# Kernel tuning notes

Measured on AMD Instinct MI355X. Metric: run time of the kernel, lower is better.

The kernel has to match this reference:

```python
import jax, jax.numpy as jnp
import numpy as np

NUM_STREAMS = 4
SINKHORN_ITERS = 10
TAU = 0.05


def sinkhorn_project(logits):
    # logits: [S, S] -> near doubly-stochastic matrix, log-domain Sinkhorn
    S = logits.shape[0]
    scaled = logits / TAU
    scaled = scaled - jnp.max(scaled)
    log_marginal = jnp.full((S,), -jnp.log(jnp.asarray(S, scaled.dtype)), dtype=scaled.dtype)
    u = jnp.zeros((S,), dtype=scaled.dtype)
    v = jnp.zeros((S,), dtype=scaled.dtype)

    def body(_, uv):
        u, v = uv
        u = log_marginal - jax.nn.logsumexp(scaled + v[None, :], axis=1)
        v = log_marginal - jax.nn.logsumexp(scaled + u[:, None], axis=0)
        return (u, v)

    u, v = jax.lax.fori_loop(0, SINKHORN_ITERS, body, (u, v))
    return jnp.exp(scaled + u[:, None] + v[None, :]) * S


def setup_inputs() -> dict:
    key = jax.random.key(0)
    k1, k2, k3, k4 = jax.random.split(key, 4)
    B_eff, T, D = 32, 2048, 1024  # B_eff = B * NUM_STREAMS
    streams = jax.random.normal(k1, (B_eff, T, D), dtype=jnp.float32)
    # params initialized like the module (base logit scale 8.0)
    base = 8.0
    h_res_logits = jnp.full((NUM_STREAMS, NUM_STREAMS), -base, dtype=jnp.float32)
    h_res_logits = h_res_logits.at[jnp.arange(NUM_STREAMS), jnp.arange(NUM_STREAMS)].set(0.0)
    h_res_logits = h_res_logits + 0.1 * jax.random.normal(k2, (NUM_STREAMS, NUM_STREAMS), dtype=jnp.float32)
    h_pre_logits = jnp.full((NUM_STREAMS,), -base, dtype=jnp.float32).at[0].set(0.0)
    h_pre_logits = h_pre_logits + 0.1 * jax.random.normal(k3, (NUM_STREAMS,), dtype=jnp.float32)
    h_post_logits = jnp.full((NUM_STREAMS,), -base, dtype=jnp.float32).at[0].set(0.0)
    h_post_logits = h_post_logits + 0.1 * jax.random.normal(k4, (NUM_STREAMS,), dtype=jnp.float32)
    return {"streams": streams, "h_res_logits": h_res_logits,
            "h_pre_logits": h_pre_logits, "h_post_logits": h_post_logits}


def reference(streams, h_res_logits, h_pre_logits, h_post_logits):
    S = NUM_STREAMS
    BS, T, D = streams.shape
    B = BS // S
    # [B*S, T, D] -> [B, T, S, D]
    x = streams.reshape(B, S, T, D).transpose(0, 2, 1, 3)
    h_res = sinkhorn_project(h_res_logits)           # [S, S]
    h_pre = jax.nn.softmax(h_pre_logits)             # [S]
    h_post = jax.nn.softmax(h_post_logits)           # [S]
    residual_mixed = jnp.einsum('ij,btjd->btid', h_res, x)   # [B, T, S, D]
    branch_input = jnp.einsum('s,btsd->btd', h_pre, x)       # [B, T, D]
    branch_output = branch_input  # branch_fn = identity
    out = residual_mixed + branch_output[:, :, None, :] * h_post[None, None, :, None]
    # [B, T, S, D] -> [B*S, T, D]
    return out.transpose(0, 2, 1, 3).reshape(B * S, T, D)
```

## Files before the change

### kernel.cpp

```cpp
#include <hip/hip_runtime.h>
#include <math.h>

#define NSTREAMS 4
#define SINKHORN_ITERS 10
#define TAU 0.05f
#define BATCH 8
#define N4_SHIFT 19
#define TOTAL_ITEMS (BATCH << N4_SHIFT)

typedef float f32x4 __attribute__((ext_vector_type(4)));

__global__ void coeff_kernel(const float* __restrict__ res_logits,
                             const float* __restrict__ pre_logits,
                             const float* __restrict__ post_logits,
                             float* __restrict__ coeffs) {
    if (threadIdx.x != 0 || blockIdx.x != 0) return;

    float scaled[NSTREAMS][NSTREAMS];
    float mx = -INFINITY;
    #pragma unroll
    for (int i = 0; i < NSTREAMS; ++i)
        #pragma unroll
        for (int j = 0; j < NSTREAMS; ++j) {
            float sv = res_logits[i * NSTREAMS + j] * (1.0f / TAU);
            scaled[i][j] = sv;
            mx = fmaxf(mx, sv);
        }
    #pragma unroll
    for (int i = 0; i < NSTREAMS; ++i)
        #pragma unroll
        for (int j = 0; j < NSTREAMS; ++j)
            scaled[i][j] -= mx;

    const float logm = -logf((float)NSTREAMS);
    float uu[NSTREAMS] = {0.f, 0.f, 0.f, 0.f};
    float vv[NSTREAMS] = {0.f, 0.f, 0.f, 0.f};

    for (int it = 0; it < SINKHORN_ITERS; ++it) {
        #pragma unroll
        for (int i = 0; i < NSTREAMS; ++i) {
            float m = -INFINITY;
            #pragma unroll
            for (int j = 0; j < NSTREAMS; ++j) m = fmaxf(m, scaled[i][j] + vv[j]);
            float s = 0.f;
            #pragma unroll
            for (int j = 0; j < NSTREAMS; ++j) s += expf(scaled[i][j] + vv[j] - m);
            uu[i] = logm - (m + logf(s));
        }
        #pragma unroll
        for (int j = 0; j < NSTREAMS; ++j) {
            float m = -INFINITY;
            #pragma unroll
            for (int i = 0; i < NSTREAMS; ++i) m = fmaxf(m, scaled[i][j] + uu[i]);
            float s = 0.f;
            #pragma unroll
            for (int i = 0; i < NSTREAMS; ++i) s += expf(scaled[i][j] + uu[i] - m);
            vv[j] = logm - (m + logf(s));
        }
    }
    #pragma unroll
    for (int i = 0; i < NSTREAMS; ++i)
        #pragma unroll
        for (int j = 0; j < NSTREAMS; ++j)
            coeffs[i * NSTREAMS + j] =
                expf(scaled[i][j] + uu[i] + vv[j]) * (float)NSTREAMS;

    {
        float m = -INFINITY;
        #pragma unroll
        for (int k = 0; k < NSTREAMS; ++k) m = fmaxf(m, pre_logits[k]);
        float e[NSTREAMS], s = 0.f;
        #pragma unroll
        for (int k = 0; k < NSTREAMS; ++k) { e[k] = expf(pre_logits[k] - m); s += e[k]; }
        #pragma unroll
        for (int k = 0; k < NSTREAMS; ++k) coeffs[16 + k] = e[k] / s;
    }
    {
        float m = -INFINITY;
        #pragma unroll
        for (int k = 0; k < NSTREAMS; ++k) m = fmaxf(m, post_logits[k]);
        float e[NSTREAMS], s = 0.f;
        #pragma unroll
        for (int k = 0; k < NSTREAMS; ++k) { e[k] = expf(post_logits[k] - m); s += e[k]; }
        #pragma unroll
        for (int k = 0; k < NSTREAMS; ++k) coeffs[20 + k] = e[k] / s;
    }
}

__global__ __launch_bounds__(256) void mix_kernel(const f32x4* __restrict__ in,
                                                  f32x4* __restrict__ out,
                                                  const float* __restrict__ coeffs) {
    float hres[16], hpre[4], hpost[4];
    #pragma unroll
    for (int k = 0; k < 16; ++k) hres[k] = coeffs[k];
    #pragma unroll
    for (int k = 0; k < 4; ++k) { hpre[k] = coeffs[16 + k]; hpost[k] = coeffs[20 + k]; }

    const int stride = gridDim.x * blockDim.x;
    for (int p = blockIdx.x * blockDim.x + threadIdx.x; p < TOTAL_ITEMS; p += stride) {
        const int b = p >> N4_SHIFT;
        const int r = p & ((1 << N4_SHIFT) - 1);
        const int base = (b << 2) << N4_SHIFT;

        const f32x4 x0 = __builtin_nontemporal_load(&in[base + (0 << N4_SHIFT) + r]);
        const f32x4 x1 = __builtin_nontemporal_load(&in[base + (1 << N4_SHIFT) + r]);
        const f32x4 x2 = __builtin_nontemporal_load(&in[base + (2 << N4_SHIFT) + r]);
        const f32x4 x3 = __builtin_nontemporal_load(&in[base + (3 << N4_SHIFT) + r]);

        f32x4 bi = hpre[0] * x0;
        bi += hpre[1] * x1;
        bi += hpre[2] * x2;
        bi += hpre[3] * x3;

        #pragma unroll
        for (int i = 0; i < 4; ++i) {
            f32x4 o = hres[i * 4 + 0] * x0;
            o += hres[i * 4 + 1] * x1;
            o += hres[i * 4 + 2] * x2;
            o += hres[i * 4 + 3] * x3;
            o += hpost[i] * bi;
            __builtin_nontemporal_store(o, &out[base + (i << N4_SHIFT) + r]);
        }
    }
}

extern "C" void kernel_launch(void* const* d_in, const int* in_sizes, int n_in,
                              void* d_out, int out_size, void* d_ws, size_t ws_size,
                              hipStream_t stream) {
    const float* streams     = (const float*)d_in[0];
    const float* h_res_log   = (const float*)d_in[1];
    const float* h_pre_log   = (const float*)d_in[2];
    const float* h_post_log  = (const float*)d_in[3];
    float* out    = (float*)d_out;
    float* coeffs = (float*)d_ws;

    coeff_kernel<<<1, 64, 0, stream>>>(h_res_log, h_pre_log, h_post_log, coeffs);

    const int block = 256;
    const int grid  = 2048;
    mix_kernel<<<grid, block, 0, stream>>>((const f32x4*)streams, (f32x4*)out, coeffs);
}
```

Before: 462.6 us.

## Fuse Sinkhorn coefficient computation into the mix kernel per block

Removes the separate single-thread coefficient kernel: each block now computes the Sinkhorn projection with four lanes using shuffles, and the pre/post softmaxes on another lane, then shares the results via LDS. The mix loop is also restructured so each thread owns one position r and walks all 8 batches, with unroll 2, instead of a grid-stride loop. This drops one kernel launch and its dependency gap, at the cost of redundant per-block coefficient work and a __syncthreads before streaming starts.

```diff
diff --git a/kernel.cpp b/kernel.cpp
--- a/kernel.cpp
+++ b/kernel.cpp
@@ -6,100 +6,101 @@
 #define TAU 0.05f
 #define BATCH 8
 #define N4_SHIFT 19
-#define TOTAL_ITEMS (BATCH << N4_SHIFT)
 
 typedef float f32x4 __attribute__((ext_vector_type(4)));
 
-__global__ void coeff_kernel(const float* __restrict__ res_logits,
-                             const float* __restrict__ pre_logits,
-                             const float* __restrict__ post_logits,
-                             float* __restrict__ coeffs) {
-    if (threadIdx.x != 0 || blockIdx.x != 0) return;
+__global__ __launch_bounds__(256) void fused_mix_kernel(
+    const f32x4* __restrict__ in,
+    f32x4* __restrict__ out,
+    const float* __restrict__ res_logits,
+    const float* __restrict__ pre_logits,
+    const float* __restrict__ post_logits)
+{
+    __shared__ float sc[24];
 
-    float scaled[NSTREAMS][NSTREAMS];
-    float mx = -INFINITY;
-    #pragma unroll
-    for (int i = 0; i < NSTREAMS; ++i)
+    const int tid = threadIdx.x;
+
+    if (tid < 4) {
+        const int l = tid;
+        float row[4], col[4];
+        float mx = -INFINITY;
         #pragma unroll
-        for (int j = 0; j < NSTREAMS; ++j) {
-            float sv = res_logits[i * NSTREAMS + j] * (1.0f / TAU);
-            scaled[i][j] = sv;
-            mx = fmaxf(mx, sv);
+        for (int j = 0; j < 4; ++j) {
+            row[j] = res_logits[l * 4 + j] * (1.0f / TAU);
+            mx = fmaxf(mx, row[j]);
         }
-    #pragma unroll
-    for (int i = 0; i < NSTREAMS; ++i)
+        {
+            const float m0 = __shfl(mx, 0), m1 = __shfl(mx, 1);
+            const float m2 = __shfl(mx, 2), m3 = __shfl(mx, 3);
+            mx = fmaxf(fmaxf(m0, m1), fmaxf(m2, m3));
+        }
         #pragma unroll
-        for (int j = 0; j < NSTREAMS; ++j)
-            scaled[i][j] -= mx;
+        for (int j = 0; j < 4; ++j) row[j] -= mx;
+        #pragma unroll
+        for (int i = 0; i < 4; ++i) col[i] = res_logits[i * 4 + l] * (1.0f / TAU) - mx;
 
-    const float logm = -logf((float)NSTREAMS);
-    float uu[NSTREAMS] = {0.f, 0.f, 0.f, 0.f};
-    float vv[NSTREAMS] = {0.f, 0.f, 0.f, 0.f};
+        const float logm = -logf((float)NSTREAMS);
+        float u_l = 0.f, v_l = 0.f;
+        float u_all[4], v_all[4] = {0.f, 0.f, 0.f, 0.f};
 
-    for (int it = 0; it < SINKHORN_ITERS; ++it) {
-        #pragma unroll
-        for (int i = 0; i < NSTREAMS; ++i) {
+        for (int it = 0; it < SINKHORN_ITERS; ++it) {
             float m = -INFINITY;
             #pragma unroll
-            for (int j = 0; j < NSTREAMS; ++j) m = fmaxf(m, scaled[i][j] + vv[j]);
+            for (int j = 0; j < 4; ++j) m = fmaxf(m, row[j] + v_all[j]);
             float s = 0.f;
             #pragma unroll
-            for (int j = 0; j < NSTREAMS; ++j) s += expf(scaled[i][j] + vv[j] - m);
-            uu[i] = logm - (m + logf(s));
+            for (int j = 0; j < 4; ++j) s += expf(row[j] + v_all[j] - m);
+            u_l = logm - (m + logf(s));
+            u_all[0] = __shfl(u_l, 0); u_all[1] = __shfl(u_l, 1);
+            u_all[2] = __shfl(u_l, 2); u_all[3] = __shfl(u_l, 3);
+
+            m = -INFINITY;
+            #pragma unroll
+            for (int i = 0; i < 4; ++i) m = fmaxf(m, col[i] + u_all[i]);
+            s = 0.f;
+            #pragma unroll
+            for (int i = 0; i < 4; ++i) s += expf(col[i] + u_all[i] - m);
+            v_l = logm - (m + logf(s));
+            v_all[0] = __shfl(v_l, 0); v_all[1] = __shfl(v_l, 1);
+            v_all[2] = __shfl(v_l, 2); v_all[3] = __shfl(v_l, 3);
         }
         #pragma unroll
-        for (int j = 0; j < NSTREAMS; ++j) {
+        for (int i = 0; i < 4; ++i)
+            sc[i * 4 + l] = expf(col[i] + u_all[i] + v_l) * (float)NSTREAMS;
+    } else if (tid == 64) {
+        {
             float m = -INFINITY;
             #pragma unroll
-            for (int i = 0; i < NSTREAMS; ++i) m = fmaxf(m, scaled[i][j] + uu[i]);
-            float s = 0.f;
+            for (int k = 0; k < 4; ++k) m = fmaxf(m, pre_logits[k]);
+            float e[4], s = 0.f;
             #pragma unroll
-            for (int i = 0; i < NSTREAMS; ++i) s += expf(scaled[i][j] + uu[i] - m);
-            vv[j] = logm - (m + logf(s));
+            for (int k = 0; k < 4; ++k) { e[k] = expf(pre_logits[k] - m); s += e[k]; }
+            #pragma unroll
+            for (int k = 0; k < 4; ++k) sc[16 + k] = e[k] / s;
+        }
+        {
+            float m = -INFINITY;
+            #pragma unroll
+            for (int k = 0; k < 4; ++k) m = fmaxf(m, post_logits[k]);
+            float e[4], s = 0.f;
+            #pragma unroll
+            for (int k = 0; k < 4; ++k) { e[k] = expf(post_logits[k] - m); s += e[k]; }
+            #pragma unroll
+            for (int k = 0; k < 4; ++k) sc[20 + k] = e[k] / s;
         }
     }
-    #pragma unroll
-    for (int i = 0; i < NSTREAMS; ++i)
-        #pragma unroll
-        for (int j = 0; j < NSTREAMS; ++j)
-            coeffs[i * NSTREAMS + j] =
-                expf(scaled[i][j] + uu[i] + vv[j]) * (float)NSTREAMS;
+    __syncthreads();
 
-    {
-        float m = -INFINITY;
-        #pragma unroll
-        for (int k = 0; k < NSTREAMS; ++k) m = fmaxf(m, pre_logits[k]);
-        float e[NSTREAMS], s = 0.f;
-        #pragma unroll
-        for (int k = 0; k < NSTREAMS; ++k) { e[k] = expf(pre_logits[k] - m); s += e[k]; }
-        #pragma unroll
-        for (int k = 0; k < NSTREAMS; ++k) coeffs[16 + k] = e[k] / s;
-    }
-    {
-        float m = -INFINITY;
-        #pragma unroll
-        for (int k = 0; k < NSTREAMS; ++k) m = fmaxf(m, post_logits[k]);
-        float e[NSTREAMS], s = 0.f;
-        #pragma unroll
-        for (int k = 0; k < NSTREAMS; ++k) { e[k] = expf(post_logits[k] - m); s += e[k]; }
-        #pragma unroll
-        for (int k = 0; k < NSTREAMS; ++k) coeffs[20 + k] = e[k] / s;
-    }
-}
-
-__global__ __launch_bounds__(256) void mix_kernel(const f32x4* __restrict__ in,
-                                                  f32x4* __restrict__ out,
-                                                  const float* __restrict__ coeffs) {
     float hres[16], hpre[4], hpost[4];
     #pragma unroll
-    for (int k = 0; k < 16; ++k) hres[k] = coeffs[k];
+    for (int k = 0; k < 16; ++k) hres[k] = sc[k];
     #pragma unroll
-    for (int k = 0; k < 4; ++k) { hpre[k] = coeffs[16 + k]; hpost[k] = coeffs[20 + k]; }
+    for (int k = 0; k < 4; ++k) { hpre[k] = sc[16 + k]; hpost[k] = sc[20 + k]; }
 
-    const int stride = gridDim.x * blockDim.x;
-    for (int p = blockIdx.x * blockDim.x + threadIdx.x; p < TOTAL_ITEMS; p += stride) {
-        const int b = p >> N4_SHIFT;
-        const int r = p & ((1 << N4_SHIFT) - 1);
+    const int r = blockIdx.x * blockDim.x + tid;
+
+    #pragma unroll 2
+    for (int b = 0; b < BATCH; ++b) {
         const int base = (b << 2) << N4_SHIFT;
 
         const f32x4 x0 = __builtin_nontemporal_load(&in[base + (0 << N4_SHIFT) + r]);
@@ -131,12 +132,8 @@
     const float* h_res_log   = (const float*)d_in[1];
     const float* h_pre_log   = (const float*)d_in[2];
     const float* h_post_log  = (const float*)d_in[3];
-    float* out    = (float*)d_out;
-    float* coeffs = (float*)d_ws;
+    float* out = (float*)d_out;
 
-    coeff_kernel<<<1, 64, 0, stream>>>(h_res_log, h_pre_log, h_post_log, coeffs);
-
-    const int block = 256;
-    const int grid  = 2048;
-    mix_kernel<<<grid, block, 0, stream>>>((const f32x4*)streams, (f32x4*)out, coeffs);
+    fused_mix_kernel<<<2048, 256, 0, stream>>>(
+        (const f32x4*)streams, (f32x4*)out, h_res_log, h_pre_log, h_post_log);
 }
```

New measurement: 461.5 us. About the same (-0.2%).

## Fold pre/post mixing into one 4x4 matrix and launch one thread per item

Applied to the files above, without the earlier changes.

Precomputes M = h_res + outer(h_post, h_pre) in the coefficient kernel, so the mixing kernel does a single 4x4 matrix-vector product per element instead of a separate branch-input reduction. It also replaces the grid-stride loop with a grid sized to one item per thread, and uses ordinary loads and stores instead of nontemporal ones. The kernel is memory-bound, so the arithmetic savings matter little. Dropping the nontemporal hints changes how the streamed data is cached, and the larger grid adds block scheduling overhead.

```diff
diff --git a/kernel.cpp b/kernel.cpp
--- a/kernel.cpp
+++ b/kernel.cpp
@@ -4,16 +4,15 @@
 #define NSTREAMS 4
 #define SINKHORN_ITERS 10
 #define TAU 0.05f
-#define BATCH 8
 #define N4_SHIFT 19
-#define TOTAL_ITEMS (BATCH << N4_SHIFT)
+#define TOTAL_ITEMS (8 << N4_SHIFT)
 
 typedef float f32x4 __attribute__((ext_vector_type(4)));
 
 __global__ void coeff_kernel(const float* __restrict__ res_logits,
                              const float* __restrict__ pre_logits,
                              const float* __restrict__ post_logits,
-                             float* __restrict__ coeffs) {
+                             float* __restrict__ Mout) {
     if (threadIdx.x != 0 || blockIdx.x != 0) return;
 
     float scaled[NSTREAMS][NSTREAMS];
@@ -58,13 +57,15 @@
             vv[j] = logm - (m + logf(s));
         }
     }
+
+    float hres[NSTREAMS][NSTREAMS];
     #pragma unroll
     for (int i = 0; i < NSTREAMS; ++i)
         #pragma unroll
         for (int j = 0; j < NSTREAMS; ++j)
-            coeffs[i * NSTREAMS + j] =
-                expf(scaled[i][j] + uu[i] + vv[j]) * (float)NSTREAMS;
+            hres[i][j] = expf(scaled[i][j] + uu[i] + vv[j]) * (float)NSTREAMS;
 
+    float hpre[NSTREAMS], hpost[NSTREAMS];
     {
         float m = -INFINITY;
         #pragma unroll
@@ -73,7 +74,7 @@
         #pragma unroll
         for (int k = 0; k < NSTREAMS; ++k) { e[k] = expf(pre_logits[k] - m); s += e[k]; }
         #pragma unroll
-        for (int k = 0; k < NSTREAMS; ++k) coeffs[16 + k] = e[k] / s;
+        for (int k = 0; k < NSTREAMS; ++k) hpre[k] = e[k] / s;
     }
     {
         float m = -INFINITY;
@@ -83,44 +84,40 @@
         #pragma unroll
         for (int k = 0; k < NSTREAMS; ++k) { e[k] = expf(post_logits[k] - m); s += e[k]; }
         #pragma unroll
-        for (int k = 0; k < NSTREAMS; ++k) coeffs[20 + k] = e[k] / s;
+        for (int k = 0; k < NSTREAMS; ++k) hpost[k] = e[k] / s;
     }
+
+    #pragma unroll
+    for (int i = 0; i < NSTREAMS; ++i)
+        #pragma unroll
+        for (int j = 0; j < NSTREAMS; ++j)
+            Mout[i * NSTREAMS + j] = hres[i][j] + hpost[i] * hpre[j];
 }
 
 __global__ __launch_bounds__(256) void mix_kernel(const f32x4* __restrict__ in,
                                                   f32x4* __restrict__ out,
-                                                  const float* __restrict__ coeffs) {
-    float hres[16], hpre[4], hpost[4];
+                                                  const float* __restrict__ M) {
+    float m[16];
     #pragma unroll
-    for (int k = 0; k < 16; ++k) hres[k] = coeffs[k];
+    for (int k = 0; k < 16; ++k) m[k] = M[k];
+
+    const int p = blockIdx.x * 256 + threadIdx.x;
+    const int b = p >> N4_SHIFT;
+    const int r = p & ((1 << N4_SHIFT) - 1);
+    const int base = (b << 2) << N4_SHIFT;
+
+    const f32x4 x0 = in[base + (0 << N4_SHIFT) + r];
+    const f32x4 x1 = in[base + (1 << N4_SHIFT) + r];
+    const f32x4 x2 = in[base + (2 << N4_SHIFT) + r];
+    const f32x4 x3 = in[base + (3 << N4_SHIFT) + r];
+
     #pragma unroll
-    for (int k = 0; k < 4; ++k) { hpre[k] = coeffs[16 + k]; hpost[k] = coeffs[20 + k]; }
-
-    const int stride = gridDim.x * blockDim.x;
-    for (int p = blockIdx.x * blockDim.x + threadIdx.x; p < TOTAL_ITEMS; p += stride) {
-        const int b = p >> N4_SHIFT;
-        const int r = p & ((1 << N4_SHIFT) - 1);
-        const int base = (b << 2) << N4_SHIFT;
-
-        const f32x4 x0 = __builtin_nontemporal_load(&in[base + (0 << N4_SHIFT) + r]);
-        const f32x4 x1 = __builtin_nontemporal_load(&in[base + (1 << N4_SHIFT) + r]);
-        const f32x4 x2 = __builtin_nontemporal_load(&in[base + (2 << N4_SHIFT) + r]);
-        const f32x4 x3 = __builtin_nontemporal_load(&in[base + (3 << N4_SHIFT) + r]);
-
-        f32x4 bi = hpre[0] * x0;
-        bi += hpre[1] * x1;
-        bi += hpre[2] * x2;
-        bi += hpre[3] * x3;
-
-        #pragma unroll
-        for (int i = 0; i < 4; ++i) {
-            f32x4 o = hres[i * 4 + 0] * x0;
-            o += hres[i * 4 + 1] * x1;
-            o += hres[i * 4 + 2] * x2;
-            o += hres[i * 4 + 3] * x3;
-            o += hpost[i] * bi;
-            __builtin_nontemporal_store(o, &out[base + (i << N4_SHIFT) + r]);
-        }
+    for (int i = 0; i < 4; ++i) {
+        f32x4 o = m[i * 4 + 0] * x0;
+        o += m[i * 4 + 1] * x1;
+        o += m[i * 4 + 2] * x2;
+        o += m[i * 4 + 3] * x3;
+        out[base + (i << N4_SHIFT) + r] = o;
     }
 }
 
@@ -131,12 +128,11 @@
     const float* h_res_log   = (const float*)d_in[1];
     const float* h_pre_log   = (const float*)d_in[2];
     const float* h_post_log  = (const float*)d_in[3];
-    float* out    = (float*)d_out;
-    float* coeffs = (float*)d_ws;
+    float* out = (float*)d_out;
+    float* M   = (float*)d_ws;
 
-    coeff_kernel<<<1, 64, 0, stream>>>(h_res_log, h_pre_log, h_post_log, coeffs);
+    coeff_kernel<<<1, 64, 0, stream>>>(h_res_log, h_pre_log, h_post_log, M);
 
-    const int block = 256;
-    const int grid  = 2048;
-    mix_kernel<<<grid, block, 0, stream>>>((const f32x4*)streams, (f32x4*)out, coeffs);
+    mix_kernel<<<TOTAL_ITEMS / 256, 256, 0, stream>>>(
+        (const f32x4*)streams, (f32x4*)out, M);
 }
```

After: 460.1 us. No clear change (-0.5%).
